# Kernel optimization log

Measured on AMD Instinct MI355X. Metric: run time of the kernel, lower is better.

The kernel has to match this reference:

```python
import jax, jax.numpy as jnp
import numpy as np

I, O, R = 64, 64, 896          # input / output / regulatory protein counts
N = I + O + R                  # total GRN size
WARMUP = 25                    # warmup_count


def setup_inputs() -> dict:
    key = jax.random.key(0)
    k1, k2, k3, k4 = jax.random.split(key, 4)
    return {
        "inputs": jax.random.uniform(k1, (16384, I), dtype=jnp.float32),
        "identifiers": jax.random.uniform(k2, (N,), dtype=jnp.float32),
        "enhancers": jax.random.uniform(k3, (N,), dtype=jnp.float32),
        "inhibitors": jax.random.uniform(k4, (N,), dtype=jnp.float32),
        "beta": jnp.full((1,), 2.0, dtype=jnp.float32),
        "delta": jnp.full((1,), 1.0, dtype=jnp.float32),
    }


def _signatures(identifiers, enhancers, inhibitors, beta):
    # sig[j, i] = exp(-beta * |tag_j - id_i|): affinity of protein j regulating protein i.
    enh = jnp.exp(-beta * jnp.abs(enhancers[:, None] - identifiers[None, :]))
    inh = jnp.exp(-beta * jnp.abs(inhibitors[:, None] - identifiers[None, :]))
    # output proteins do not regulate others -> zero their rows
    mask = jnp.ones((N,), dtype=enh.dtype).at[I:I + O].set(0.0)[:, None]
    return enh * mask, inh * mask


def _step(conc, sig_diff, delta):
    # conc: [..., N]; sig_diff = enh_sigs - inh_sigs: [N, N]
    dc = (delta / N) * (conc @ sig_diff)
    new = jnp.maximum(conc + dc, 0.0)
    reg = new[..., I:]                                    # outputs + regulatory
    s = jnp.sum(reg, axis=-1, keepdims=True)
    reg = jnp.where(s > 0, reg / s, reg)                  # renormalize
    return jnp.concatenate([conc[..., :I], reg], axis=-1)  # inputs clamped


def reference(inputs, identifiers, enhancers, inhibitors, beta, delta):
    b, d = beta[0], delta[0]
    enh_s, inh_s = _signatures(identifiers, enhancers, inhibitors, b)
    sig_diff = enh_s - inh_s

    # setup(): uniform initial concentrations; warmup(): shared sequential steps
    conc0 = jnp.full((N,), 1.0 / N, dtype=jnp.float32)
    def warm(c, _):
        return _step(c, sig_diff, d), None
    conc, _ = jax.lax.scan(warm, conc0, None, length=WARMUP)

    # per-sample (batched instead of tf.map_fn): set input concs, one step
    B = inputs.shape[0]
    batch_conc = jnp.concatenate(
        [inputs, jnp.broadcast_to(conc[I:], (B, N - I))], axis=-1)
    new = _step(batch_conc, sig_diff, d)
    return new[..., I:I + O]  # output protein concentrations [B, O]
```

## Files before the change

kernel.cpp:

```cpp
#include <hip/hip_runtime.h>
#include <math.h>

#define NJ 960
#define NSRC 896
#define NWARM 25

typedef unsigned long long u64;
typedef unsigned int u32;

#define RK_O 0u
#define CT_O 896u
#define HD_O 1856u
#define WK_F 8192u
#define BASE_F 69632u

#define TAG_RK 0x524B0001u
#define TAG_CT 0x43540001u
#define TAG_HD 0x48440001u

__device__ __forceinline__ void ast(u64* p, u64 v) {
  __hip_atomic_store(p, v, __ATOMIC_RELAXED, __HIP_MEMORY_SCOPE_AGENT);
}
__device__ __forceinline__ u64 ald(const u64* p) {
  return __hip_atomic_load(p, __ATOMIC_RELAXED, __HIP_MEMORY_SCOPE_AGENT);
}
__device__ __forceinline__ u32 poll32(const u64* p, u32 tag) {
  u64 v = ald(p);
  while ((u32)(v >> 32) != tag) { __builtin_amdgcn_s_sleep(1); v = ald(p); }
  return (u32)v;
}

__global__ __launch_bounds__(256) void front_k(const float* __restrict__ ident,
                                               const float* __restrict__ enh,
                                               const float* __restrict__ inh,
                                               const float* __restrict__ beta,
                                               const float* __restrict__ delta,
                                               void* __restrict__ wsv) {
  u64* RK = (u64*)wsv + RK_O;
  u64* CT = (u64*)wsv + CT_O;
  u64* HD = (u64*)wsv + HD_O;
  float* Wk = (float*)wsv + WK_F;
  float* base = (float*)wsv + BASE_F;

  const int tid = threadIdx.x;
  const float bb = beta[0];
  const float dN = delta[0] / 1024.0f;

  if (blockIdx.x > 30) {
    const int g2 = (int)(blockIdx.x - 31) * 256 + tid;
    int k = g2 / 120;
    int jb = (g2 % 120) * 8;
    float ek = enh[k], ik = inh[k];
    #pragma unroll
    for (int u = 0; u < 8; ++u) {
      float cj = ident[64 + jb + u];
      Wk[(size_t)k * NJ + jb + u] =
          dN * (expf(-bb * fabsf(ek - cj)) - expf(-bb * fabsf(ik - cj)));
    }
    return;
  }

  if (blockIdx.x > 0) {
    const int g = (int)(blockIdx.x - 1) * 256 + tid;
    const int c8 = g & 7;
    if (g < NSRC * 8) {
      int m = g >> 3;
      float myE = enh[128 + m], myI = inh[128 + m];
      int re = 0, ri = 0;
      for (int i = 112 * c8; i < 112 * c8 + 112; ++i) {
        float ev = enh[128 + i], iv = inh[128 + i];
        re += (ev < myE || (ev == myE && i < m)) ? 1 : 0;
        ri += (iv < myI || (iv == myI && i < m)) ? 1 : 0;
      }
      int p = re | (ri << 16);
      p += __shfl_xor(p, 1); p += __shfl_xor(p, 2); p += __shfl_xor(p, 4);
      if (c8 == 0) ast(&RK[m], ((u64)TAG_RK << 32) | (u32)p);
    }
    {
      int j = g >> 3;
      float cj = ident[64 + j];
      int ce = 0, ci = 0;
      for (int i = 112 * c8; i < 112 * c8 + 112; ++i) {
        ce += (enh[128 + i] <= cj) ? 1 : 0;
        ci += (inh[128 + i] <= cj) ? 1 : 0;
      }
      int p = ce | (ci << 16);
      p += __shfl_xor(p, 1); p += __shfl_xor(p, 2); p += __shfl_xor(p, 4);
      if (c8 == 0) ast(&CT[j], ((u64)TAG_CT << 32) | (u32)p);
    }
    {
      int j = g >> 3;
      float cj = ident[64 + j];
      float h = 0.0f;
      for (int k = 8 * c8; k < 8 * c8 + 8; ++k)
        h += expf(-bb * fabsf(enh[k] - cj)) - expf(-bb * fabsf(inh[k] - cj));
      h += __shfl_xor(h, 1); h += __shfl_xor(h, 2); h += __shfl_xor(h, 4);
      if (c8 == 0)
        ast(&HD[j], ((u64)TAG_HD << 32) |
                    (u64)__float_as_uint(dN * h * (1.0f / 1024.0f)));
    }
    return;
  }

  __shared__ float yl[NJ];
  __shared__ float2 scanE[1024];
  __shared__ float2 scanI[1024];
  __shared__ float4 wtot[4];
  __shared__ float ssw[4];

  const int lane = tid & 63, wvid = tid >> 6;

  int rE[4], rI[4];
  if (tid < 224) {
    #pragma unroll
    for (int s = 0; s < 4; ++s) {
      u32 v = poll32(&RK[4 * tid + s], TAG_RK);
      rE[s] = v & 0xFFFF; rI[s] = v >> 16;
    }
  }
  int cE[4], cI[4];
  float hd[4], fm[4], fp[4];
  if (tid < 240) {
    #pragma unroll
    for (int c = 0; c < 4; ++c) {
      u32 v = poll32(&CT[4 * tid + c], TAG_CT);
      cE[c] = v & 0xFFFF; cI[c] = v >> 16;
      hd[c] = __uint_as_float(poll32(&HD[4 * tid + c], TAG_HD));
      float cj = ident[64 + 4 * tid + c];
      fm[c] = expf(-bb * cj); fp[c] = expf(bb * cj);
    }
  }
  float EP[4], EN[4], IP[4], IN2[4];
  if (tid < 224) {
    #pragma unroll
    for (int s = 0; s < 4; ++s) {
      float e = enh[128 + 4 * tid + s], i2 = inh[128 + 4 * tid + s];
      EP[s] = expf(bb * e);  EN[s] = expf(-bb * e);
      IP[s] = expf(bb * i2); IN2[s] = expf(-bb * i2);
    }
  }
  float y_own[4] = {1.0f / 1024.0f, 1.0f / 1024.0f, 1.0f / 1024.0f, 1.0f / 1024.0f};
  if (tid < 240) {
    #pragma unroll
    for (int c = 0; c < 4; ++c) yl[4 * tid + c] = 1.0f / 1024.0f;
  }
  __syncthreads();

  for (int t = 0; t <= NWARM; ++t) {
    if (tid == 0) {
      scanE[0] = make_float2(0.f, 0.f);
      scanI[0] = make_float2(0.f, 0.f);
    }
    if (tid >= 224) {
      #pragma unroll
      for (int c = 0; c < 4; ++c) {
        int p = 4 * tid + c;
        if (p > NSRC) {
          scanE[p] = make_float2(0.f, 0.f);
          scanI[p] = make_float2(0.f, 0.f);
        }
      }
    }
    if (tid < 224) {
      #pragma unroll
      for (int s = 0; s < 4; ++s) {
        float ym = yl[64 + 4 * tid + s];
        scanE[rE[s] + 1] = make_float2(ym * EP[s], ym * EN[s]);
        scanI[rI[s] + 1] = make_float2(ym * IP[s], ym * IN2[s]);
      }
    }
    __syncthreads();

    float2 e0 = scanE[4 * tid], e1 = scanE[4 * tid + 1],
           e2 = scanE[4 * tid + 2], e3 = scanE[4 * tid + 3];
    float2 i0 = scanI[4 * tid], i1 = scanI[4 * tid + 1],
           i2v = scanI[4 * tid + 2], i3 = scanI[4 * tid + 3];
    e1.x += e0.x; e1.y += e0.y; e2.x += e1.x; e2.y += e1.y; e3.x += e2.x; e3.y += e2.y;
    i1.x += i0.x; i1.y += i0.y; i2v.x += i1.x; i2v.y += i1.y; i3.x += i2v.x; i3.y += i2v.y;
    float4 tot = make_float4(e3.x, e3.y, i3.x, i3.y);
    float4 inc = tot;
    #pragma unroll
    for (int off = 1; off < 64; off <<= 1) {
      float ox = __shfl_up(inc.x, off, 64);
      float oy = __shfl_up(inc.y, off, 64);
      float oz = __shfl_up(inc.z, off, 64);
      float ow = __shfl_up(inc.w, off, 64);
      if (lane >= off) { inc.x += ox; inc.y += oy; inc.z += oz; inc.w += ow; }
    }
    if (lane == 63) wtot[wvid] = inc;
    __syncthreads();
    float4 exc = make_float4(inc.x - tot.x, inc.y - tot.y,
                             inc.z - tot.z, inc.w - tot.w);
    #pragma unroll
    for (int w = 0; w < 3; ++w)
      if (w < wvid) {
        float4 p = wtot[w];
        exc.x += p.x; exc.y += p.y; exc.z += p.z; exc.w += p.w;
      }
    e0.x += exc.x; e0.y += exc.y; e1.x += exc.x; e1.y += exc.y;
    e2.x += exc.x; e2.y += exc.y; e3.x += exc.x; e3.y += exc.y;
    i0.x += exc.z; i0.y += exc.w; i1.x += exc.z; i1.y += exc.w;
    i2v.x += exc.z; i2v.y += exc.w; i3.x += exc.z; i3.y += exc.w;
    scanE[4 * tid] = e0; scanE[4 * tid + 1] = e1;
    scanE[4 * tid + 2] = e2; scanE[4 * tid + 3] = e3;
    scanI[4 * tid] = i0; scanI[4 * tid + 1] = i1;
    scanI[4 * tid + 2] = i2v; scanI[4 * tid + 3] = i3;
    __syncthreads();

    float nv[4] = {0.f, 0.f, 0.f, 0.f};
    float psum = 0.0f;
    if (tid < 240) {
      float2 TE = scanE[NSRC], TI = scanI[NSRC];
      #pragma unroll
      for (int c = 0; c < 4; ++c) {
        float2 AE = scanE[cE[c]], AI = scanI[cI[c]];
        float dot = fm[c] * AE.x + fp[c] * (TE.y - AE.y)
                  - fm[c] * AI.x - fp[c] * (TI.y - AI.y);
        float pre = y_own[c] + dN * dot;
        if (t < NWARM) {
          nv[c] = fmaxf(pre + hd[c], 0.0f);
          psum += nv[c];
        } else {
          base[4 * tid + c] = pre;
        }
      }
    }
    if (t < NWARM) {
      #pragma unroll
      for (int off = 32; off >= 1; off >>= 1) psum += __shfl_xor(psum, off);
      if (lane == 0) ssw[wvid] = psum;
      __syncthreads();
      float s = ssw[0] + ssw[1] + ssw[2] + ssw[3];
      float inv = (s > 0.0f) ? 1.0f / s : 1.0f;
      if (tid < 240) {
        #pragma unroll
        for (int c = 0; c < 4; ++c) {
          y_own[c] = nv[c] * inv;
          yl[4 * tid + c] = y_own[c];
        }
      }
    }
    __syncthreads();
  }
}

__global__ __launch_bounds__(512) void batch_k(const float* __restrict__ inp,
                                               const float* __restrict__ ws,
                                               float* __restrict__ out) {
  __shared__ float At[64][36];
  __shared__ float Wl[16][512];
  __shared__ float bch[NJ];

  const int tid = threadIdx.x;
  const int colg = tid & 63;
  const int rowg = tid >> 6;
  const size_t rowbase = (size_t)blockIdx.x * 32;
  const float* __restrict__ Wk = ws + WK_F;

  {
    int r = tid >> 4, c4 = (tid & 15) * 4;
    float4 f4 = *(const float4*)(inp + (rowbase + r) * 64 + c4);
    At[c4 + 0][r] = f4.x; At[c4 + 1][r] = f4.y;
    At[c4 + 2][r] = f4.z; At[c4 + 3][r] = f4.w;
  }
  if (tid < 240) {
    float4 b4 = *(const float4*)(ws + BASE_F + 4 * tid);
    bch[4 * tid + 0] = b4.x; bch[4 * tid + 1] = b4.y;
    bch[4 * tid + 2] = b4.z; bch[4 * tid + 3] = b4.w;
  }

  float acc[4][8];
  float rs[4] = {0.f, 0.f, 0.f, 0.f};

  #pragma unroll 1
  for (int ch = 0; ch < 2; ++ch) {
    const int c0 = ch ? 0 : 512;

    #pragma unroll
    for (int r = 0; r < 4; ++r)
      #pragma unroll
      for (int c = 0; c < 8; ++c) acc[r][c] = 0.0f;

    #pragma unroll 1
    for (int s = 0; s < 4; ++s) {
      __syncthreads();
      #pragma unroll
      for (int i = 0; i < 4; ++i) {
        int fi = tid + i * 512;
        int kk = fi >> 7;
        int c4 = (fi & 127) * 4;
        int j = c0 + c4;
        float4 v = make_float4(0.f, 0.f, 0.f, 0.f);
        if (j < NJ)
          v = *(const float4*)(Wk + (size_t)(16 * s + kk) * NJ + j);
        *(float4*)&Wl[kk][c4] = v;
      }
      __syncthreads();
      #pragma unroll
      for (int kk = 0; kk < 16; ++kk) {
        float4 av = *(const float4*)&At[16 * s + kk][rowg * 4];
        float4 w0 = *(const float4*)&Wl[kk][colg * 4];
        float4 w1 = *(const float4*)&Wl[kk][256 + colg * 4];
        float a_[4] = {av.x, av.y, av.z, av.w};
        float w_[8] = {w0.x, w0.y, w0.z, w0.w, w1.x, w1.y, w1.z, w1.w};
        #pragma unroll
        for (int r = 0; r < 4; ++r)
          #pragma unroll
          for (int c = 0; c < 8; ++c)
            acc[r][c] = fmaf(a_[r], w_[c], acc[r][c]);
      }
    }

    #pragma unroll
    for (int c = 0; c < 8; ++c) {
      int cl = (c < 4) ? (colg * 4 + c) : (256 + colg * 4 + (c - 4));
      int j = c0 + cl;
      float bv = (j < NJ) ? bch[j] : -1.0e30f;
      #pragma unroll
      for (int r = 0; r < 4; ++r)
        rs[r] += fmaxf(acc[r][c] + bv, 0.0f);
    }
  }

  #pragma unroll
  for (int r = 0; r < 4; ++r) {
    float v = rs[r];
    #pragma unroll
    for (int off = 32; off >= 1; off >>= 1) v += __shfl_xor(v, off);
    rs[r] = v;
  }
  if (colg < 16) {
    #pragma unroll
    for (int r = 0; r < 4; ++r) {
      float inv = (rs[r] > 0.0f) ? 1.0f / rs[r] : 1.0f;
      float* op = out + (rowbase + rowg * 4 + r) * 64 + colg * 4;
      float4 o;
      o.x = fmaxf(acc[r][0] + bch[colg * 4 + 0], 0.0f) * inv;
      o.y = fmaxf(acc[r][1] + bch[colg * 4 + 1], 0.0f) * inv;
      o.z = fmaxf(acc[r][2] + bch[colg * 4 + 2], 0.0f) * inv;
      o.w = fmaxf(acc[r][3] + bch[colg * 4 + 3], 0.0f) * inv;
      *(float4*)op = o;
    }
  }
}

extern "C" void kernel_launch(void* const* d_in, const int* in_sizes, int n_in,
                              void* d_out, int out_size, void* d_ws, size_t ws_size,
                              hipStream_t stream) {
  const float* inp   = (const float*)d_in[0];
  const float* ident = (const float*)d_in[1];
  const float* enh   = (const float*)d_in[2];
  const float* inh   = (const float*)d_in[3];
  const float* beta  = (const float*)d_in[4];
  const float* delta = (const float*)d_in[5];

  hipLaunchKernelGGL(front_k, dim3(61), dim3(256), 0, stream,
                     ident, enh, inh, beta, delta, d_ws);
  hipLaunchKernelGGL(batch_k, dim3(512), dim3(512), 0, stream,
                     inp, (const float*)d_ws, (float*)d_out);
}
```

Baseline: 155.1 us.

## Run warmup recurrence in a single wavefront to eliminate block barriers

The 25-step warmup loop of the front kernel now runs in one 64-lane wavefront, with each lane owning 15 proteins in registers. Transposed shared-memory scan buffers and a wave-only shuffle scan replace the four-wave scan and its __syncthreads barriers. Explicit lgkmcnt waits handle ordering within the wave. The polling sleep interval also grows. This removes per-step block-level synchronisation on the serial critical path, at the cost of more serial work per lane and higher register pressure.

```diff
diff --git a/kernel.cpp b/kernel.cpp
--- a/kernel.cpp
+++ b/kernel.cpp
@@ -26,16 +26,18 @@
 }
 __device__ __forceinline__ u32 poll32(const u64* p, u32 tag) {
   u64 v = ald(p);
-  while ((u32)(v >> 32) != tag) { __builtin_amdgcn_s_sleep(1); v = ald(p); }
+  while ((u32)(v >> 32) != tag) { __builtin_amdgcn_s_sleep(8); v = ald(p); }
   return (u32)v;
 }
 
-__global__ __launch_bounds__(256) void front_k(const float* __restrict__ ident,
-                                               const float* __restrict__ enh,
-                                               const float* __restrict__ inh,
-                                               const float* __restrict__ beta,
-                                               const float* __restrict__ delta,
-                                               void* __restrict__ wsv) {
+__global__ __launch_bounds__(256, 1) void front_k(
+    const float* __restrict__ ident, const float* __restrict__ enh,
+    const float* __restrict__ inh, const float* __restrict__ beta,
+    const float* __restrict__ delta, void* __restrict__ wsv) {
+  __shared__ float2 SE[16][64];
+  __shared__ float2 SI[16][64];
+  __shared__ float4 SRCX[NSRC];
+
   u64* RK = (u64*)wsv + RK_O;
   u64* CT = (u64*)wsv + CT_O;
   u64* HD = (u64*)wsv + HD_O;
@@ -102,83 +104,66 @@
     return;
   }
 
-  __shared__ float yl[NJ];
-  __shared__ float2 scanE[1024];
-  __shared__ float2 scanI[1024];
-  __shared__ float4 wtot[4];
-  __shared__ float ssw[4];
-
-  const int lane = tid & 63, wvid = tid >> 6;
-
-  int rE[4], rI[4];
-  if (tid < 224) {
-    #pragma unroll
-    for (int s = 0; s < 4; ++s) {
-      u32 v = poll32(&RK[4 * tid + s], TAG_RK);
-      rE[s] = v & 0xFFFF; rI[s] = v >> 16;
-    }
-  }
-  int cE[4], cI[4];
-  float hd[4], fm[4], fp[4];
-  if (tid < 240) {
-    #pragma unroll
-    for (int c = 0; c < 4; ++c) {
-      u32 v = poll32(&CT[4 * tid + c], TAG_CT);
-      cE[c] = v & 0xFFFF; cI[c] = v >> 16;
-      hd[c] = __uint_as_float(poll32(&HD[4 * tid + c], TAG_HD));
-      float cj = ident[64 + 4 * tid + c];
-      fm[c] = expf(-bb * cj); fp[c] = expf(bb * cj);
-    }
-  }
-  float EP[4], EN[4], IP[4], IN2[4];
-  if (tid < 224) {
-    #pragma unroll
-    for (int s = 0; s < 4; ++s) {
-      float e = enh[128 + 4 * tid + s], i2 = inh[128 + 4 * tid + s];
-      EP[s] = expf(bb * e);  EN[s] = expf(-bb * e);
-      IP[s] = expf(bb * i2); IN2[s] = expf(-bb * i2);
-    }
-  }
-  float y_own[4] = {1.0f / 1024.0f, 1.0f / 1024.0f, 1.0f / 1024.0f, 1.0f / 1024.0f};
-  if (tid < 240) {
-    #pragma unroll
-    for (int c = 0; c < 4; ++c) yl[4 * tid + c] = 1.0f / 1024.0f;
-  }
-  __syncthreads();
+  if (tid >= 64) return;
+  const int lane = tid;
+
+  for (int m = lane; m < NSRC; m += 64) {
+    float e = enh[128 + m], iv = inh[128 + m];
+    SRCX[m] = make_float4(expf(bb * e), expf(-bb * e),
+                          expf(bb * iv), expf(-bb * iv));
+  }
+  #pragma unroll
+  for (int u = 0; u < 16; ++u) {
+    SE[u][lane] = make_float2(0.f, 0.f);
+    SI[u][lane] = make_float2(0.f, 0.f);
+  }
+  asm volatile("s_waitcnt lgkmcnt(0)" ::: "memory");
+  __builtin_amdgcn_sched_barrier(0);
+
+  const int c0l = lane * 15;
+  float fmv[15], fpv[15], hdv[15], y[15];
+  int cc[15], rr[15];
+  #pragma unroll
+  for (int s = 0; s < 15; ++s) {
+    float cj = ident[64 + c0l + s];
+    fmv[s] = expf(-bb * cj); fpv[s] = expf(bb * cj);
+    y[s] = 1.0f / 1024.0f;
+    rr[s] = 0;
+  }
+  #pragma unroll
+  for (int s = 0; s < 15; ++s) {
+    cc[s] = (int)poll32(&CT[c0l + s], TAG_CT);
+    hdv[s] = __uint_as_float(poll32(&HD[c0l + s], TAG_HD));
+  }
+  #pragma unroll
+  for (int s = 0; s < 15; ++s) {
+    int c = c0l + s;
+    if (c >= 64) rr[s] = (int)poll32(&RK[c - 64], TAG_RK);
+  }
 
   for (int t = 0; t <= NWARM; ++t) {
-    if (tid == 0) {
-      scanE[0] = make_float2(0.f, 0.f);
-      scanI[0] = make_float2(0.f, 0.f);
-    }
-    if (tid >= 224) {
-      #pragma unroll
-      for (int c = 0; c < 4; ++c) {
-        int p = 4 * tid + c;
-        if (p > NSRC) {
-          scanE[p] = make_float2(0.f, 0.f);
-          scanI[p] = make_float2(0.f, 0.f);
-        }
-      }
-    }
-    if (tid < 224) {
-      #pragma unroll
-      for (int s = 0; s < 4; ++s) {
-        float ym = yl[64 + 4 * tid + s];
-        scanE[rE[s] + 1] = make_float2(ym * EP[s], ym * EN[s]);
-        scanI[rI[s] + 1] = make_float2(ym * IP[s], ym * IN2[s]);
-      }
-    }
-    __syncthreads();
-
-    float2 e0 = scanE[4 * tid], e1 = scanE[4 * tid + 1],
-           e2 = scanE[4 * tid + 2], e3 = scanE[4 * tid + 3];
-    float2 i0 = scanI[4 * tid], i1 = scanI[4 * tid + 1],
-           i2v = scanI[4 * tid + 2], i3 = scanI[4 * tid + 3];
-    e1.x += e0.x; e1.y += e0.y; e2.x += e1.x; e2.y += e1.y; e3.x += e2.x; e3.y += e2.y;
-    i1.x += i0.x; i1.y += i0.y; i2v.x += i1.x; i2v.y += i1.y; i3.x += i2v.x; i3.y += i2v.y;
-    float4 tot = make_float4(e3.x, e3.y, i3.x, i3.y);
-    float4 inc = tot;
+    #pragma unroll
+    for (int s = 0; s < 15; ++s) {
+      int c = c0l + s;
+      if (c >= 64) {
+        float4 X = SRCX[c - 64];
+        int qE = (rr[s] & 0xFFFF) + 1;
+        int qI = ((rr[s] >> 16) & 0xFFFF) + 1;
+        SE[qE & 15][qE >> 4] = make_float2(y[s] * X.x, y[s] * X.y);
+        SI[qI & 15][qI >> 4] = make_float2(y[s] * X.z, y[s] * X.w);
+      }
+    }
+    asm volatile("s_waitcnt lgkmcnt(0)" ::: "memory");
+    __builtin_amdgcn_sched_barrier(0);
+
+    float2 tE = make_float2(0.f, 0.f), tI = make_float2(0.f, 0.f);
+    #pragma unroll
+    for (int u = 0; u < 16; ++u) {
+      float2 a = SE[u][lane], b = SI[u][lane];
+      tE.x += a.x; tE.y += a.y; tI.x += b.x; tI.y += b.y;
+    }
+    float4 inc = make_float4(tE.x, tE.y, tI.x, tI.y);
+    float4 tot = inc;
     #pragma unroll
     for (int off = 1; off < 64; off <<= 1) {
       float ox = __shfl_up(inc.x, off, 64);
@@ -187,60 +172,43 @@
       float ow = __shfl_up(inc.w, off, 64);
       if (lane >= off) { inc.x += ox; inc.y += oy; inc.z += oz; inc.w += ow; }
     }
-    if (lane == 63) wtot[wvid] = inc;
-    __syncthreads();
-    float4 exc = make_float4(inc.x - tot.x, inc.y - tot.y,
-                             inc.z - tot.z, inc.w - tot.w);
-    #pragma unroll
-    for (int w = 0; w < 3; ++w)
-      if (w < wvid) {
-        float4 p = wtot[w];
-        exc.x += p.x; exc.y += p.y; exc.z += p.z; exc.w += p.w;
-      }
-    e0.x += exc.x; e0.y += exc.y; e1.x += exc.x; e1.y += exc.y;
-    e2.x += exc.x; e2.y += exc.y; e3.x += exc.x; e3.y += exc.y;
-    i0.x += exc.z; i0.y += exc.w; i1.x += exc.z; i1.y += exc.w;
-    i2v.x += exc.z; i2v.y += exc.w; i3.x += exc.z; i3.y += exc.w;
-    scanE[4 * tid] = e0; scanE[4 * tid + 1] = e1;
-    scanE[4 * tid + 2] = e2; scanE[4 * tid + 3] = e3;
-    scanI[4 * tid] = i0; scanI[4 * tid + 1] = i1;
-    scanI[4 * tid + 2] = i2v; scanI[4 * tid + 3] = i3;
-    __syncthreads();
-
-    float nv[4] = {0.f, 0.f, 0.f, 0.f};
-    float psum = 0.0f;
-    if (tid < 240) {
-      float2 TE = scanE[NSRC], TI = scanI[NSRC];
-      #pragma unroll
-      for (int c = 0; c < 4; ++c) {
-        float2 AE = scanE[cE[c]], AI = scanI[cI[c]];
-        float dot = fm[c] * AE.x + fp[c] * (TE.y - AE.y)
-                  - fm[c] * AI.x - fp[c] * (TI.y - AI.y);
-        float pre = y_own[c] + dN * dot;
-        if (t < NWARM) {
-          nv[c] = fmaxf(pre + hd[c], 0.0f);
-          psum += nv[c];
-        } else {
-          base[4 * tid + c] = pre;
-        }
+    float TEy = __shfl(inc.y, 63, 64);
+    float TIy = __shfl(inc.w, 63, 64);
+    float2 pe = make_float2(inc.x - tot.x, inc.y - tot.y);
+    float2 pi = make_float2(inc.z - tot.z, inc.w - tot.w);
+
+    #pragma unroll
+    for (int u = 0; u < 16; ++u) {
+      float2 a = SE[u][lane], b = SI[u][lane];
+      pe.x += a.x; pe.y += a.y; pi.x += b.x; pi.y += b.y;
+      if (lane * 16 + u <= NSRC) { SE[u][lane] = pe; SI[u][lane] = pi; }
+    }
+    asm volatile("s_waitcnt lgkmcnt(0)" ::: "memory");
+    __builtin_amdgcn_sched_barrier(0);
+
+    float nv[15]; float psum = 0.0f;
+    #pragma unroll
+    for (int s = 0; s < 15; ++s) {
+      int cE = cc[s] & 0xFFFF, cI = (cc[s] >> 16) & 0xFFFF;
+      float2 AE = SE[cE & 15][cE >> 4];
+      float2 AI = SI[cI & 15][cI >> 4];
+      float dot = fmv[s] * AE.x + fpv[s] * (TEy - AE.y)
+                - fmv[s] * AI.x - fpv[s] * (TIy - AI.y);
+      float pre = y[s] + dN * dot;
+      if (t < NWARM) {
+        nv[s] = fmaxf(pre + hdv[s], 0.0f);
+        psum += nv[s];
+      } else {
+        base[c0l + s] = pre;
       }
     }
     if (t < NWARM) {
       #pragma unroll
       for (int off = 32; off >= 1; off >>= 1) psum += __shfl_xor(psum, off);
-      if (lane == 0) ssw[wvid] = psum;
-      __syncthreads();
-      float s = ssw[0] + ssw[1] + ssw[2] + ssw[3];
-      float inv = (s > 0.0f) ? 1.0f / s : 1.0f;
-      if (tid < 240) {
-        #pragma unroll
-        for (int c = 0; c < 4; ++c) {
-          y_own[c] = nv[c] * inv;
-          yl[4 * tid + c] = y_own[c];
-        }
-      }
-    }
-    __syncthreads();
+      float invs = (psum > 0.0f) ? 1.0f / psum : 1.0f;
+      #pragma unroll
+      for (int s = 0; s < 15; ++s) y[s] = nv[s] * invs;
+    }
   }
 }
 
```

Result: slower. 185.3 us (+19.5%).
